# Kernel tuning notes

Hardware: AMD Instinct MI355X
Metric: run time of the kernel (lower is better)

The kernel has to match this reference:

```python
import jax, jax.numpy as jnp
import numpy as np

N_EMBED = 1024
N_HEADS = 16
HEAD_SIZE = N_EMBED // N_HEADS
B, T = 4, 2048
LN_EPS = 1e-5


def _layer_norm(x, gamma, beta):
    mu = jnp.mean(x, axis=-1, keepdims=True)
    var = jnp.var(x, axis=-1, keepdims=True)
    return (x - mu) * jax.lax.rsqrt(var + LN_EPS) * gamma + beta


def setup_inputs() -> dict:
    key = jax.random.key(0)
    ks = jax.random.split(key, 12)
    s = 1.0 / np.sqrt(N_EMBED)
    sh = 1.0 / np.sqrt(4 * N_EMBED)
    return {
        "x": jax.random.normal(ks[0], (B, T, N_EMBED), jnp.float32),
        "Wk": jax.random.uniform(ks[1], (N_EMBED, N_EMBED), jnp.float32, -s, s),
        "Wq": jax.random.uniform(ks[2], (N_EMBED, N_EMBED), jnp.float32, -s, s),
        "Wv": jax.random.uniform(ks[3], (N_EMBED, N_EMBED), jnp.float32, -s, s),
        "Wproj": jax.random.uniform(ks[4], (N_EMBED, N_EMBED), jnp.float32, -s, s),
        "bproj": jax.random.uniform(ks[5], (N_EMBED,), jnp.float32, -s, s),
        "W1": jax.random.uniform(ks[6], (N_EMBED, 4 * N_EMBED), jnp.float32, -s, s),
        "b1": jax.random.uniform(ks[7], (4 * N_EMBED,), jnp.float32, -s, s),
        "W2": jax.random.uniform(ks[8], (4 * N_EMBED, N_EMBED), jnp.float32, -sh, sh),
        "b2": jax.random.uniform(ks[9], (N_EMBED,), jnp.float32, -sh, sh),
        "g1": jnp.ones((N_EMBED,), jnp.float32),
        "beta1": jnp.zeros((N_EMBED,), jnp.float32),
        "g2": jnp.ones((N_EMBED,), jnp.float32),
        "beta2": jnp.zeros((N_EMBED,), jnp.float32),
    }


def reference(x, Wk, Wq, Wv, Wproj, bproj, W1, b1, W2, b2, g1, beta1, g2, beta2):
    Bt, Tt, C = x.shape
    h = _layer_norm(x, g1, beta1)
    # project and split heads: (B, H, T, D)
    def heads(W):
        return (h @ W).reshape(Bt, Tt, N_HEADS, HEAD_SIZE).transpose(0, 2, 1, 3)
    q, k, v = heads(Wq), heads(Wk), heads(Wv)
    wei = jnp.einsum("bhtd,bhsd->bhts", q, k) / np.sqrt(HEAD_SIZE)
    causal = jnp.tril(jnp.ones((Tt, Tt), bool))
    wei = jnp.where(causal, wei, -jnp.inf)
    wei = jax.nn.softmax(wei, axis=-1)
    out = jnp.einsum("bhts,bhsd->bhtd", wei, v)
    out = out.transpose(0, 2, 1, 3).reshape(Bt, Tt, C)
    x = x + out @ Wproj + bproj
    h2 = _layer_norm(x, g2, beta2)
    ff = jax.nn.relu(h2 @ W1 + b1) @ W2 + b2
    return x + ff
```

## Files before the change

### kernel.cpp

```cpp
#include <hip/hip_runtime.h>
#include <stdint.h>

typedef __bf16 bf16x8 __attribute__((ext_vector_type(8)));
typedef float f32x4 __attribute__((ext_vector_type(4)));
typedef unsigned short u16x8 __attribute__((ext_vector_type(8)));
typedef unsigned short u16x4 __attribute__((ext_vector_type(4)));
typedef unsigned int u32x2 __attribute__((ext_vector_type(2)));
typedef float fvec4 __attribute__((ext_vector_type(4)));

__device__ __forceinline__ unsigned short f2b(float f) {
  unsigned u = __builtin_bit_cast(unsigned, f);
  return (unsigned short)((u + 0x7fffu + ((u >> 16) & 1u)) >> 16);
}

__device__ __forceinline__ bf16x8 ldfrag(const unsigned short* p) {
  return __builtin_bit_cast(bf16x8, *(const u16x8*)p);
}

__device__ __forceinline__ float fexp2(float x) {
  float r;
  asm("v_exp_f32 %0, %1" : "=v"(r) : "v"(x));
  return r;
}

__device__ __forceinline__ unsigned cvtpk(float a, float b) {
  unsigned r;
  asm("v_cvt_pk_bf16_f32 %0, %1, %2" : "=v"(r) : "v"(a), "v"(b));
  return r;
}

__device__ __forceinline__ void gload_lds16(const void* g, void* l) {
  auto gp = reinterpret_cast<const __attribute__((address_space(1))) void*>(
      reinterpret_cast<uintptr_t>(g));
  auto lp = reinterpret_cast<__attribute__((address_space(3))) void*>(
      reinterpret_cast<uintptr_t>(l));
  __builtin_amdgcn_global_load_lds(gp, lp, 16, 0, 0);
}

__global__ void transpose_cast(const float* __restrict__ W, unsigned short* __restrict__ Wt,
                               int K, int N) {
  __shared__ float tile[32][33];
  const int n0 = blockIdx.x * 32, k0 = blockIdx.y * 32;
  const int tx = threadIdx.x, ty = threadIdx.y;
#pragma unroll
  for (int j = 0; j < 4; ++j)
    tile[ty + j * 8][tx] = W[(size_t)(k0 + ty + j * 8) * N + n0 + tx];
  __syncthreads();
#pragma unroll
  for (int j = 0; j < 4; ++j)
    Wt[(size_t)(n0 + ty + j * 8) * K + k0 + tx] = f2b(tile[tx][ty + j * 8]);
}

__global__ void ln_kernel(const float* __restrict__ X, const float* __restrict__ g,
                          const float* __restrict__ be, unsigned short* __restrict__ H) {
  const int row = (blockIdx.x * blockDim.x + threadIdx.x) >> 6;
  const int l = threadIdx.x & 63;
  const float* xr = X + (size_t)row * 1024;
  fvec4 v[4];
  float s = 0.f, sq = 0.f;
#pragma unroll
  for (int i = 0; i < 4; ++i) {
    v[i] = *(const fvec4*)(xr + i * 256 + l * 4);
#pragma unroll
    for (int j = 0; j < 4; ++j) { s += v[i][j]; sq += v[i][j] * v[i][j]; }
  }
#pragma unroll
  for (int off = 32; off >= 1; off >>= 1) {
    s += __shfl_xor(s, off);
    sq += __shfl_xor(sq, off);
  }
  const float mean = s * (1.f / 1024.f);
  const float var = sq * (1.f / 1024.f) - mean * mean;
  const float rstd = rsqrtf(var + 1e-5f);
#pragma unroll
  for (int i = 0; i < 4; ++i) {
    const int col = i * 256 + l * 4;
    fvec4 gg = *(const fvec4*)(g + col);
    fvec4 bb = *(const fvec4*)(be + col);
    u16x4 o;
#pragma unroll
    for (int j = 0; j < 4; ++j) o[j] = f2b((v[i][j] - mean) * rstd * gg[j] + bb[j]);
    *(u16x4*)(H + (size_t)row * 1024 + col) = o;
  }
}

template <int BM, int BN, int WM, int WN, int NBUF, int NTH, int EPI>
__global__ __launch_bounds__(NTH, 2) void gemm8p(
    const unsigned short* __restrict__ A, const unsigned short* __restrict__ Bt,
    const float* __restrict__ bias, const float* __restrict__ resid,
    float* __restrict__ Cf, unsigned short* __restrict__ Cb,
    unsigned short* __restrict__ pK, unsigned short* __restrict__ pVT,
    int M, int N, int K, int ntiles) {
  constexpr int BK = 32;
  constexpr int ASZ = BM * BK * 2;
  constexpr int BSZ = BN * BK * 2;
  constexpr int BUFSZ = ASZ + BSZ;
  constexpr int NW = NTH / 64;
  static_assert(WM * WN == NW, "wave grid");
  constexpr int MF = BM / (WM * 16);
  constexpr int NF = BN / (WN * 16);
  constexpr int UA = ASZ / (NTH * 16);
  constexpr int UB = BSZ / (NTH * 16);
  constexpr int UNITS = UA + UB;
  constexpr int VMSTEADY = (NBUF - 2) * UNITS;
  static_assert(UA * NTH * 16 == ASZ && UB * NTH * 16 == BSZ, "unit split");
  __shared__ __align__(16) char lds[NBUF * BUFSZ];

  const int tid = threadIdx.x;
  const int w = tid >> 6, l = tid & 63;
  const int wr = w / WN, wc = w % WN;
  const int kg = l >> 4, fr = l & 15;
  const int xtiles = N / BN;
  const int nblk = (int)gridDim.x;

  int Aoff[MF], Boff[NF];
#pragma unroll
  for (int m = 0; m < MF; ++m) {
    const int r = wr * (MF * 16) + m * 16 + fr;
    Aoff[m] = r * 64 + ((kg * 16) ^ (((r >> 1) & 3) << 4));
  }
#pragma unroll
  for (int n = 0; n < NF; ++n) {
    const int r = wc * (NF * 16) + n * 16 + fr;
    Boff[n] = ASZ + r * 64 + ((kg * 16) ^ (((r >> 1) & 3) << 4));
  }

  for (int tl = (int)blockIdx.x; tl < ntiles; tl += nblk) {
    if (tl != (int)blockIdx.x) __builtin_amdgcn_s_barrier();
    const int q8 = ntiles >> 3;
    const int swz = (tl & 7) * q8 + (tl >> 3);
    const size_t am0 = (size_t)(swz / xtiles) * BM;
    const size_t bn0 = (size_t)(swz % xtiles) * BN;

    const char* src[UNITS];
#pragma unroll
    for (int u = 0; u < UA; ++u) {
      const int flatq = u * NTH + tid;
      const int row = flatq >> 2;
      const int scb = ((flatq & 3) << 4) ^ (((row >> 1) & 3) << 4);
      src[u] = (const char*)(A + (am0 + row) * K) + scb;
    }
#pragma unroll
    for (int u = 0; u < UB; ++u) {
      const int flatq = u * NTH + tid;
      const int row = flatq >> 2;
      const int scb = ((flatq & 3) << 4) ^ (((row >> 1) & 3) << 4);
      src[UA + u] = (const char*)(Bt + (bn0 + row) * K) + scb;
    }

    f32x4 acc[MF][NF];
#pragma unroll
    for (int m = 0; m < MF; ++m)
#pragma unroll
      for (int n = 0; n < NF; ++n) acc[m][n] = (f32x4){0.f, 0.f, 0.f, 0.f};

    auto stage = [&](int sb) {
#pragma unroll
      for (int u = 0; u < UNITS; ++u) {
        gload_lds16(src[u], lds + sb * BUFSZ + u * (NTH * 16) + tid * 16);
        src[u] += 64;
      }
    };

    const int NT = K / BK;
#pragma unroll
    for (int p = 0; p < NBUF - 1; ++p) stage(p);
    asm volatile("s_waitcnt vmcnt(%0)" ::"i"(VMSTEADY) : "memory");
    __builtin_amdgcn_s_barrier();

    int cb0 = 0, sb = NBUF - 1;
    for (int kt = 0; kt < NT; ++kt) {
      if (kt + NBUF - 1 < NT) stage(sb);
      bf16x8 af[MF], bf[NF];
#pragma unroll
      for (int m = 0; m < MF; ++m)
        af[m] = ldfrag((const unsigned short*)(lds + cb0 + Aoff[m]));
#pragma unroll
      for (int n = 0; n < NF; ++n)
        bf[n] = ldfrag((const unsigned short*)(lds + cb0 + Boff[n]));
      __builtin_amdgcn_s_setprio(1);
#pragma unroll
      for (int m = 0; m < MF; ++m)
#pragma unroll
        for (int n = 0; n < NF; ++n)
          acc[m][n] = __builtin_amdgcn_mfma_f32_16x16x32_bf16(af[m], bf[n], acc[m][n], 0, 0, 0);
      __builtin_amdgcn_s_setprio(0);
      if (kt + NBUF - 1 < NT) {
        asm volatile("s_waitcnt vmcnt(%0)" ::"i"(VMSTEADY) : "memory");
        __builtin_amdgcn_s_barrier();
      } else if (kt + 2 < NT) {
        asm volatile("s_waitcnt vmcnt(%0)" ::"i"(UNITS) : "memory");
        __builtin_amdgcn_s_barrier();
      } else if (kt + 1 < NT) {
        asm volatile("s_waitcnt vmcnt(0)" ::: "memory");
        __builtin_amdgcn_s_barrier();
      }
      cb0 += BUFSZ;
      if (cb0 == NBUF * BUFSZ) cb0 = 0;
      sb += 1;
      if (sb == NBUF) sb = 0;
    }

#pragma unroll
    for (int m = 0; m < MF; ++m) {
      const size_t row0 = am0 + wr * (MF * 16) + m * 16 + kg * 4;
#pragma unroll
      for (int n = 0; n < NF; ++n) {
        const size_t col = bn0 + wc * (NF * 16) + n * 16 + fr;
        if (EPI == 3) {
          if (bn0 < 1024) {
#pragma unroll
            for (int r = 0; r < 4; ++r) Cb[(row0 + r) * 1024 + col] = f2b(acc[m][n][r]);
          } else if (bn0 < 2048) {
#pragma unroll
            for (int r = 0; r < 4; ++r) pK[(row0 + r) * 1024 + col - 1024] = f2b(acc[m][n][r]);
          } else {
            const int c2 = (int)col - 2048;
            const int hh = c2 >> 6, dd = c2 & 63;
            const int bb = (int)(row0 >> 11), tt = (int)(row0 & 2047);
            u16x4 pv;
#pragma unroll
            for (int r = 0; r < 4; ++r) pv[r] = f2b(acc[m][n][r]);
            *(u16x4*)(pVT + (((size_t)bb * 16 + hh) * 64 + dd) * 2048 + tt) = pv;
          }
        } else {
          const float bv = (EPI >= 1) ? bias[col] : 0.f;
#pragma unroll
          for (int r = 0; r < 4; ++r) {
            const size_t idx = (row0 + r) * N + col;
            float v = acc[m][n][r] + bv;
            if (EPI == 1) v = fmaxf(v, 0.f);
            if (EPI == 2) {
              Cf[idx] = v + resid[idx];
            } else {
              Cb[idx] = f2b(v);
            }
          }
        }
      }
    }
  }
}

#define PSTR 72
#define SC2 0.18033688f
__global__ __launch_bounds__(256, 2) void attn_kernel(const unsigned short* __restrict__ Qb,
                                                      const unsigned short* __restrict__ Kb,
                                                      const unsigned short* __restrict__ VT,
                                                      unsigned short* __restrict__ ATT) {
  __shared__ __align__(16) char ldsK[3 * 8192];
  __shared__ __align__(16) unsigned short Pl[4][64 * PSTR];
  const int tid = threadIdx.x;
  const int w = tid >> 6, l = tid & 63;
  const int kg = l >> 4, fr = l & 15;
  const int bh = blockIdx.x;
  const int b = bh >> 4, h = bh & 15;
  const int yy = (int)blockIdx.y;
  const int qt = (yy < 4) ? 7 - yy : yy - 4;
  const int q0 = qt * 256 + w * 64;
  const size_t rbase = (size_t)b * 2048;
  const unsigned short* vtb = VT + (size_t)bh * 64 * 2048;
  const f32x4 fz = {0.f, 0.f, 0.f, 0.f};

  const int rowoff = tid >> 3;
  const int cbsw = ((tid & 7) * 16) ^ ((rowoff & 7) << 4);
  const char* ksrc = (const char*)(Kb + rbase * 1024 + h * 64) + (size_t)rowoff * 2048 + cbsw;

  int koff[4][2];
#pragma unroll
  for (int sg = 0; sg < 4; ++sg)
#pragma unroll
    for (int c = 0; c < 2; ++c)
      koff[sg][c] = (sg * 16 + fr) * 128 + ((c * 64 + kg * 16) ^ ((fr & 7) << 4));

  bf16x8 bq[4][2];
#pragma unroll
  for (int qg = 0; qg < 4; ++qg) {
    const unsigned short* qrow = Qb + (rbase + q0 + qg * 16 + fr) * 1024 + h * 64;
#pragma unroll
    for (int c = 0; c < 2; ++c) bq[qg][c] = ldfrag(qrow + c * 32 + kg * 8);
  }

  f32x4 o[4][4];
#pragma unroll
  for (int qg = 0; qg < 4; ++qg)
#pragma unroll
    for (int nd = 0; nd < 4; ++nd) o[qg][nd] = (f32x4){0.f, 0.f, 0.f, 0.f};
  float m_run2[4] = {-1e30f, -1e30f, -1e30f, -1e30f};
  float l_run[4] = {0.f, 0.f, 0.f, 0.f};

  auto stage = [&](int t, int sbuf) {
    gload_lds16(ksrc + (size_t)(t * 64) * 2048, ldsK + sbuf * 8192 + tid * 16);
    gload_lds16(ksrc + (size_t)(t * 64 + 32) * 2048, ldsK + sbuf * 8192 + 4096 + tid * 16);
  };

  auto softmax_qg = [&](int qg, int s0, f32x4 (&stq)[4]) -> float {
    const int qa = q0 + qg * 16 + fr;
    float vals[16];
    if (s0 + 63 <= q0 + qg * 16) {
#pragma unroll
      for (int sg = 0; sg < 4; ++sg)
#pragma unroll
        for (int r = 0; r < 4; ++r) vals[sg * 4 + r] = stq[sg][r];
    } else {
#pragma unroll
      for (int sg = 0; sg < 4; ++sg)
#pragma unroll
        for (int r = 0; r < 4; ++r) {
          const int sa = s0 + sg * 16 + kg * 4 + r;
          vals[sg * 4 + r] = (sa > qa) ? -1e30f : stq[sg][r];
        }
    }
    float m5[5];
#pragma unroll
    for (int i = 0; i < 5; ++i)
      m5[i] = fmaxf(fmaxf(vals[3 * i], vals[3 * i + 1]), vals[3 * i + 2]);
    const float vmax =
        fmaxf(fmaxf(fmaxf(m5[0], m5[1]), m5[2]), fmaxf(fmaxf(m5[3], m5[4]), vals[15]));
    const float tm2 = vmax * SC2;
    if (__any(tm2 > m_run2[qg] + 8.f)) {
      float tmax2 = tm2;
      tmax2 = fmaxf(tmax2, __shfl_xor(tmax2, 16));
      tmax2 = fmaxf(tmax2, __shfl_xor(tmax2, 32));
      const float m_new2 = fmaxf(m_run2[qg], tmax2);
      const float alpha = fexp2(m_run2[qg] - m_new2);
      m_run2[qg] = m_new2;
      l_run[qg] *= alpha;
      float al[4];
#pragma unroll
      for (int r = 0; r < 4; ++r) al[r] = __shfl(alpha, kg * 4 + r);
#pragma unroll
      for (int nd = 0; nd < 4; ++nd)
#pragma unroll
        for (int r = 0; r < 4; ++r) o[qg][nd][r] *= al[r];
    }
    const float nm2 = -m_run2[qg];
    float psum = 0.f;
    unsigned pk[8];
#pragma unroll
    for (int i = 0; i < 8; ++i) {
      const float p0 = fexp2(__builtin_fmaf(vals[2 * i], SC2, nm2));
      const float p1 = fexp2(__builtin_fmaf(vals[2 * i + 1], SC2, nm2));
      psum += p0 + p1;
      pk[i] = cvtpk(p0, p1);
    }
#pragma unroll
    for (int sg = 0; sg < 4; ++sg) {
      u32x2 w2 = {pk[2 * sg], pk[2 * sg + 1]};
      *(u32x2*)(&Pl[w][(qg * 16 + fr) * PSTR + sg * 16 + kg * 4]) = w2;
    }
    return psum;
  };

  auto compute = [&](int s0, int cbb) {
    if (s0 > q0 + 63) return;
    bf16x8 vb[4][2];
#pragma unroll
    for (int nd = 0; nd < 4; ++nd)
#pragma unroll
      for (int ks = 0; ks < 2; ++ks)
        vb[nd][ks] = ldfrag(vtb + (size_t)(nd * 16 + fr) * 2048 + s0 + ks * 32 + kg * 8);

    float psv[4];
#pragma unroll
    for (int qp = 0; qp < 2; ++qp) {
      f32x4 st[4][2];
#pragma unroll
      for (int sg = 0; sg < 4; ++sg) {
        const bf16x8 ka0 = ldfrag((const unsigned short*)(ldsK + cbb + koff[sg][0]));
        const bf16x8 ka1 = ldfrag((const unsigned short*)(ldsK + cbb + koff[sg][1]));
#pragma unroll
        for (int qh = 0; qh < 2; ++qh)
          st[sg][qh] = __builtin_amdgcn_mfma_f32_16x16x32_bf16(
              ka1, bq[qp * 2 + qh][1],
              __builtin_amdgcn_mfma_f32_16x16x32_bf16(ka0, bq[qp * 2 + qh][0], fz, 0, 0, 0),
              0, 0, 0);
      }
#pragma unroll
      for (int qh = 0; qh < 2; ++qh) {
        f32x4 stq[4];
#pragma unroll
        for (int sg = 0; sg < 4; ++sg) stq[sg] = st[sg][qh];
        psv[qp * 2 + qh] = softmax_qg(qp * 2 + qh, s0, stq);
      }
    }

    {
      float a[4], c[4];
#pragma unroll
      for (int qg = 0; qg < 4; ++qg) a[qg] = __shfl_xor(psv[qg], 16);
#pragma unroll
      for (int qg = 0; qg < 4; ++qg) psv[qg] += a[qg];
#pragma unroll
      for (int qg = 0; qg < 4; ++qg) c[qg] = __shfl_xor(psv[qg], 32);
#pragma unroll
      for (int qg = 0; qg < 4; ++qg) l_run[qg] += psv[qg] + c[qg];
    }

#pragma unroll
    for (int qg = 0; qg < 4; ++qg)
#pragma unroll
      for (int ks = 0; ks < 2; ++ks) {
        const bf16x8 pa = ldfrag(&Pl[w][(qg * 16 + fr) * PSTR + ks * 32 + kg * 8]);
#pragma unroll
        for (int nd = 0; nd < 4; ++nd)
          o[qg][nd] = __builtin_amdgcn_mfma_f32_16x16x32_bf16(pa, vb[nd][ks], o[qg][nd], 0, 0, 0);
      }
  };

  const int NT = 4 * qt + 4;
  stage(0, 0);
  stage(1, 1);
  asm volatile("s_waitcnt vmcnt(2)" ::: "memory");
  __builtin_amdgcn_s_barrier();
  int cb = 0, sb = 2;
  for (int t = 0; t < NT; ++t) {
    if (t + 2 < NT) stage(t + 2, sb);
    compute(t * 64, cb * 8192);
    if (t + 2 < NT) {
      asm volatile("s_waitcnt vmcnt(2)" ::: "memory");
      __builtin_amdgcn_s_barrier();
    } else if (t + 1 < NT) {
      asm volatile("s_waitcnt vmcnt(0)" ::: "memory");
      __builtin_amdgcn_s_barrier();
    }
    cb += 1; if (cb == 3) cb = 0;
    sb += 1; if (sb == 3) sb = 0;
  }

#pragma unroll
  for (int qg = 0; qg < 4; ++qg) {
    const float li = __builtin_amdgcn_rcpf(l_run[qg]);
    float linv[4];
#pragma unroll
    for (int r = 0; r < 4; ++r) linv[r] = __shfl(li, kg * 4 + r);
#pragma unroll
    for (int nd = 0; nd < 4; ++nd)
#pragma unroll
      for (int r = 0; r < 4; ++r) {
        const size_t row = rbase + q0 + qg * 16 + kg * 4 + r;
        ATT[row * 1024 + h * 64 + nd * 16 + fr] = f2b(o[qg][nd][r] * linv[r]);
      }
  }
}

extern "C" void kernel_launch(void* const* d_in, const int* in_sizes, int n_in, void* d_out,
                              int out_size, void* d_ws, size_t ws_size, hipStream_t stream) {
  const float* x = (const float*)d_in[0];
  const float* Wk = (const float*)d_in[1];
  const float* Wq = (const float*)d_in[2];
  const float* Wv = (const float*)d_in[3];
  const float* Wproj = (const float*)d_in[4];
  const float* bproj = (const float*)d_in[5];
  const float* W1 = (const float*)d_in[6];
  const float* b1 = (const float*)d_in[7];
  const float* W2 = (const float*)d_in[8];
  const float* b2 = (const float*)d_in[9];
  const float* g1 = (const float*)d_in[10];
  const float* beta1 = (const float*)d_in[11];
  const float* g2 = (const float*)d_in[12];
  const float* beta2 = (const float*)d_in[13];
  float* out = (float*)d_out;
  unsigned short* wsu = (unsigned short*)d_ws;

  const size_t o_qkvW = 0;
  const size_t o_projW = o_qkvW + 3072 * 1024;
  const size_t o_W1 = o_projW + 1024 * 1024;
  const size_t o_W2 = o_W1 + 4096 * 1024;
  const size_t o_H = o_W2 + 1024 * 4096;
  const size_t o_Q = o_H + (size_t)8192 * 1024;
  const size_t o_K = o_Q + (size_t)8192 * 1024;
  const size_t o_VT = o_K + (size_t)8192 * 1024;
  const size_t o_ATT = o_VT + (size_t)8192 * 1024;
  const size_t o_FF1 = o_Q;

  dim3 tpb(32, 8);
  transpose_cast<<<dim3(32, 32), tpb, 0, stream>>>(Wq, wsu + o_qkvW, 1024, 1024);
  transpose_cast<<<dim3(32, 32), tpb, 0, stream>>>(Wk, wsu + o_qkvW + 1024 * 1024, 1024, 1024);
  transpose_cast<<<dim3(32, 32), tpb, 0, stream>>>(Wv, wsu + o_qkvW + 2 * 1024 * 1024, 1024, 1024);
  transpose_cast<<<dim3(32, 32), tpb, 0, stream>>>(Wproj, wsu + o_projW, 1024, 1024);
  transpose_cast<<<dim3(128, 32), tpb, 0, stream>>>(W1, wsu + o_W1, 1024, 4096);
  transpose_cast<<<dim3(32, 128), tpb, 0, stream>>>(W2, wsu + o_W2, 4096, 1024);

  ln_kernel<<<2048, 256, 0, stream>>>(x, g1, beta1, wsu + o_H);

  gemm8p<256, 128, 2, 2, 3, 256, 3><<<512, 256, 0, stream>>>(
      wsu + o_H, wsu + o_qkvW, nullptr, nullptr, nullptr, wsu + o_Q, wsu + o_K, wsu + o_VT,
      8192, 3072, 1024, 768);

  attn_kernel<<<dim3(64, 8), 256, 0, stream>>>(wsu + o_Q, wsu + o_K, wsu + o_VT, wsu + o_ATT);

  gemm8p<128, 128, 2, 2, 3, 256, 2><<<512, 256, 0, stream>>>(
      wsu + o_ATT, wsu + o_projW, bproj, x, out, nullptr, nullptr, nullptr,
      8192, 1024, 1024, 512);

  ln_kernel<<<2048, 256, 0, stream>>>(out, g2, beta2, wsu + o_H);

  gemm8p<256, 128, 2, 2, 3, 256, 1><<<512, 256, 0, stream>>>(
      wsu + o_H, wsu + o_W1, b1, nullptr, nullptr, wsu + o_FF1, nullptr, nullptr,
      8192, 4096, 1024, 1024);

  gemm8p<128, 128, 2, 2, 3, 256, 2><<<512, 256, 0, stream>>>(
      wsu + o_FF1, wsu + o_W2, b2, out, out, nullptr, nullptr, nullptr,
      8192, 1024, 4096, 512);
}
```

Measured before the change: 351.5 us.

## Replace persistent GEMM with 512-thread double-buffered BK=64 split-phase pipeline

Replaces the templated persistent 256-thread GEMM with a fixed 128x256-tile, 8-wave kernel that uses two 48 KB LDS buffers and BK=64. Each K step is split into two half-phases, and the next tile's global-to-LDS loads are issued between the fragment reads and the MFMAs, so loads overlap compute. The grid becomes one block per tile instead of a persistent loop, and occupancy drops to one block per CU. Projection and FFN2 launch only 256 blocks, which may underfill the GPU and add wave-quantization losses.

```diff
diff --git a/kernel.cpp b/kernel.cpp
--- a/kernel.cpp
+++ b/kernel.cpp
@@ -84,157 +84,186 @@
   }
 }
 
-template <int BM, int BN, int WM, int WN, int NBUF, int NTH, int EPI>
-__global__ __launch_bounds__(NTH, 2) void gemm8p(
+template <int EPI>
+__global__ __launch_bounds__(512, 1) void gemm2p(
     const unsigned short* __restrict__ A, const unsigned short* __restrict__ Bt,
     const float* __restrict__ bias, const float* __restrict__ resid,
     float* __restrict__ Cf, unsigned short* __restrict__ Cb,
-    unsigned short* __restrict__ pK, unsigned short* __restrict__ pVT,
-    int M, int N, int K, int ntiles) {
-  constexpr int BK = 32;
-  constexpr int ASZ = BM * BK * 2;
-  constexpr int BSZ = BN * BK * 2;
-  constexpr int BUFSZ = ASZ + BSZ;
-  constexpr int NW = NTH / 64;
-  static_assert(WM * WN == NW, "wave grid");
-  constexpr int MF = BM / (WM * 16);
-  constexpr int NF = BN / (WN * 16);
-  constexpr int UA = ASZ / (NTH * 16);
-  constexpr int UB = BSZ / (NTH * 16);
-  constexpr int UNITS = UA + UB;
-  constexpr int VMSTEADY = (NBUF - 2) * UNITS;
-  static_assert(UA * NTH * 16 == ASZ && UB * NTH * 16 == BSZ, "unit split");
-  __shared__ __align__(16) char lds[NBUF * BUFSZ];
-
+    unsigned short* __restrict__ pK, unsigned short* __restrict__ pVT, int N, int K) {
+  __shared__ __align__(16) char lds[2 * 49152];
   const int tid = threadIdx.x;
   const int w = tid >> 6, l = tid & 63;
-  const int wr = w / WN, wc = w % WN;
+  const int wr = w >> 2, wc = w & 3;
   const int kg = l >> 4, fr = l & 15;
-  const int xtiles = N / BN;
-  const int nblk = (int)gridDim.x;
-
-  int Aoff[MF], Boff[NF];
-#pragma unroll
-  for (int m = 0; m < MF; ++m) {
-    const int r = wr * (MF * 16) + m * 16 + fr;
-    Aoff[m] = r * 64 + ((kg * 16) ^ (((r >> 1) & 3) << 4));
-  }
-#pragma unroll
-  for (int n = 0; n < NF; ++n) {
-    const int r = wc * (NF * 16) + n * 16 + fr;
-    Boff[n] = ASZ + r * 64 + ((kg * 16) ^ (((r >> 1) & 3) << 4));
-  }
-
-  for (int tl = (int)blockIdx.x; tl < ntiles; tl += nblk) {
-    if (tl != (int)blockIdx.x) __builtin_amdgcn_s_barrier();
-    const int q8 = ntiles >> 3;
-    const int swz = (tl & 7) * q8 + (tl >> 3);
-    const size_t am0 = (size_t)(swz / xtiles) * BM;
-    const size_t bn0 = (size_t)(swz % xtiles) * BN;
-
-    const char* src[UNITS];
-#pragma unroll
-    for (int u = 0; u < UA; ++u) {
-      const int flatq = u * NTH + tid;
-      const int row = flatq >> 2;
-      const int scb = ((flatq & 3) << 4) ^ (((row >> 1) & 3) << 4);
-      src[u] = (const char*)(A + (am0 + row) * K) + scb;
-    }
-#pragma unroll
-    for (int u = 0; u < UB; ++u) {
-      const int flatq = u * NTH + tid;
-      const int row = flatq >> 2;
-      const int scb = ((flatq & 3) << 4) ^ (((row >> 1) & 3) << 4);
-      src[UA + u] = (const char*)(Bt + (bn0 + row) * K) + scb;
-    }
-
-    f32x4 acc[MF][NF];
-#pragma unroll
-    for (int m = 0; m < MF; ++m)
-#pragma unroll
-      for (int n = 0; n < NF; ++n) acc[m][n] = (f32x4){0.f, 0.f, 0.f, 0.f};
-
-    auto stage = [&](int sb) {
-#pragma unroll
-      for (int u = 0; u < UNITS; ++u) {
-        gload_lds16(src[u], lds + sb * BUFSZ + u * (NTH * 16) + tid * 16);
-        src[u] += 64;
-      }
-    };
-
-    const int NT = K / BK;
-#pragma unroll
-    for (int p = 0; p < NBUF - 1; ++p) stage(p);
-    asm volatile("s_waitcnt vmcnt(%0)" ::"i"(VMSTEADY) : "memory");
+  const int ntiles = (int)gridDim.x;
+
+  const int q8 = ntiles >> 3;
+  const int bid = (int)blockIdx.x;
+  const int swz = (bid & 7) * q8 + (bid >> 3);
+  const size_t am0 = (size_t)(swz % 64) * 128;
+  const size_t bn0 = (size_t)(swz / 64) * 256;
+
+  int Aoff[2][4], Boff[2][4];
+#pragma unroll
+  for (int kk = 0; kk < 2; ++kk) {
+#pragma unroll
+    for (int mf = 0; mf < 4; ++mf) {
+      const int r = wr * 64 + mf * 16 + fr;
+      Aoff[kk][mf] = (kk ? 24576 : 0) + r * 64 + ((kg ^ ((r >> 1) & 3)) << 4);
+    }
+#pragma unroll
+    for (int nf = 0; nf < 4; ++nf) {
+      const int rn = wc * 64 + nf * 16 + fr;
+      Boff[kk][nf] = (kk ? 32768 : 8192) + rn * 64 + ((kg ^ ((rn >> 1) & 3)) << 4);
+    }
+  }
+
+  const int rA = tid >> 2, cA = tid & 3;
+  const char* sA = (const char*)(A + (am0 + rA) * K) + ((cA ^ ((rA >> 1) & 3)) << 4);
+  const int rB0 = tid >> 2;
+  const int rB1 = 128 + (tid >> 2);
+  const char* sB0 = (const char*)(Bt + (bn0 + rB0) * K) + ((cA ^ ((rB0 >> 1) & 3)) << 4);
+  const char* sB1 = (const char*)(Bt + (bn0 + rB1) * K) + ((cA ^ ((rB1 >> 1) & 3)) << 4);
+
+  f32x4 acc[4][4];
+#pragma unroll
+  for (int m = 0; m < 4; ++m)
+#pragma unroll
+    for (int n = 0; n < 4; ++n) acc[m][n] = (f32x4){0.f, 0.f, 0.f, 0.f};
+
+  const int NT = K >> 6;
+
+  auto stage_p12 = [&](int d) {
+    char* Ld = lds + d * 49152;
+    gload_lds16(sA, Ld + tid * 16);
+    gload_lds16(sB0, Ld + 8192 + tid * 16);
+    gload_lds16(sB1, Ld + 16384 + tid * 16);
+  };
+  auto stage_p34 = [&](int d) {
+    char* Ld = lds + d * 49152;
+    gload_lds16(sA + 64, Ld + 24576 + tid * 16);
+    gload_lds16(sB0 + 64, Ld + 32768 + tid * 16);
+    gload_lds16(sB1 + 64, Ld + 40960 + tid * 16);
+  };
+
+  auto do_mfma = [&](int d, int kk) {
+    const char* Ld = lds + d * 49152;
+    bf16x8 af[4], bf[4];
+#pragma unroll
+    for (int mf = 0; mf < 4; ++mf)
+      af[mf] = ldfrag((const unsigned short*)(Ld + Aoff[kk][mf]));
+#pragma unroll
+    for (int nf = 0; nf < 4; ++nf)
+      bf[nf] = ldfrag((const unsigned short*)(Ld + Boff[kk][nf]));
     __builtin_amdgcn_s_barrier();
-
-    int cb0 = 0, sb = NBUF - 1;
-    for (int kt = 0; kt < NT; ++kt) {
-      if (kt + NBUF - 1 < NT) stage(sb);
-      bf16x8 af[MF], bf[NF];
-#pragma unroll
-      for (int m = 0; m < MF; ++m)
-        af[m] = ldfrag((const unsigned short*)(lds + cb0 + Aoff[m]));
-#pragma unroll
-      for (int n = 0; n < NF; ++n)
-        bf[n] = ldfrag((const unsigned short*)(lds + cb0 + Boff[n]));
+    asm volatile("s_waitcnt lgkmcnt(0)" ::: "memory");
+    __builtin_amdgcn_sched_barrier(0);
+    __builtin_amdgcn_s_setprio(1);
+#pragma unroll
+    for (int m = 0; m < 4; ++m)
+#pragma unroll
+      for (int n = 0; n < 4; ++n)
+        acc[m][n] = __builtin_amdgcn_mfma_f32_16x16x32_bf16(af[m], bf[n], acc[m][n], 0, 0, 0);
+    __builtin_amdgcn_s_setprio(0);
+  };
+
+  stage_p12(0);
+  stage_p34(0);
+  sA += 128; sB0 += 128; sB1 += 128;
+  asm volatile("s_waitcnt vmcnt(3)" ::: "memory");
+  __builtin_amdgcn_s_barrier();
+
+  for (int t = 0; t < NT - 1; ++t) {
+    const int d = t & 1, dn = d ^ 1;
+    {
+      const char* Ld = lds + d * 49152;
+      bf16x8 af[4], bf[4];
+#pragma unroll
+      for (int mf = 0; mf < 4; ++mf)
+        af[mf] = ldfrag((const unsigned short*)(Ld + Aoff[0][mf]));
+#pragma unroll
+      for (int nf = 0; nf < 4; ++nf)
+        bf[nf] = ldfrag((const unsigned short*)(Ld + Boff[0][nf]));
+      stage_p12(dn);
+      __builtin_amdgcn_s_barrier();
+      asm volatile("s_waitcnt lgkmcnt(0)" ::: "memory");
+      __builtin_amdgcn_sched_barrier(0);
       __builtin_amdgcn_s_setprio(1);
 #pragma unroll
-      for (int m = 0; m < MF; ++m)
-#pragma unroll
-        for (int n = 0; n < NF; ++n)
+      for (int m = 0; m < 4; ++m)
+#pragma unroll
+        for (int n = 0; n < 4; ++n)
           acc[m][n] = __builtin_amdgcn_mfma_f32_16x16x32_bf16(af[m], bf[n], acc[m][n], 0, 0, 0);
       __builtin_amdgcn_s_setprio(0);
-      if (kt + NBUF - 1 < NT) {
-        asm volatile("s_waitcnt vmcnt(%0)" ::"i"(VMSTEADY) : "memory");
-        __builtin_amdgcn_s_barrier();
-      } else if (kt + 2 < NT) {
-        asm volatile("s_waitcnt vmcnt(%0)" ::"i"(UNITS) : "memory");
-        __builtin_amdgcn_s_barrier();
-      } else if (kt + 1 < NT) {
-        asm volatile("s_waitcnt vmcnt(0)" ::: "memory");
-        __builtin_amdgcn_s_barrier();
-      }
-      cb0 += BUFSZ;
-      if (cb0 == NBUF * BUFSZ) cb0 = 0;
-      sb += 1;
-      if (sb == NBUF) sb = 0;
-    }
-
-#pragma unroll
-    for (int m = 0; m < MF; ++m) {
-      const size_t row0 = am0 + wr * (MF * 16) + m * 16 + kg * 4;
-#pragma unroll
-      for (int n = 0; n < NF; ++n) {
-        const size_t col = bn0 + wc * (NF * 16) + n * 16 + fr;
-        if (EPI == 3) {
-          if (bn0 < 1024) {
-#pragma unroll
-            for (int r = 0; r < 4; ++r) Cb[(row0 + r) * 1024 + col] = f2b(acc[m][n][r]);
-          } else if (bn0 < 2048) {
-#pragma unroll
-            for (int r = 0; r < 4; ++r) pK[(row0 + r) * 1024 + col - 1024] = f2b(acc[m][n][r]);
+      asm volatile("s_waitcnt vmcnt(3)" ::: "memory");
+      __builtin_amdgcn_s_barrier();
+    }
+    {
+      const char* Ld = lds + d * 49152;
+      bf16x8 af[4], bf[4];
+#pragma unroll
+      for (int mf = 0; mf < 4; ++mf)
+        af[mf] = ldfrag((const unsigned short*)(Ld + Aoff[1][mf]));
+#pragma unroll
+      for (int nf = 0; nf < 4; ++nf)
+        bf[nf] = ldfrag((const unsigned short*)(Ld + Boff[1][nf]));
+      stage_p34(dn);
+      sA += 128; sB0 += 128; sB1 += 128;
+      __builtin_amdgcn_s_barrier();
+      asm volatile("s_waitcnt lgkmcnt(0)" ::: "memory");
+      __builtin_amdgcn_sched_barrier(0);
+      __builtin_amdgcn_s_setprio(1);
+#pragma unroll
+      for (int m = 0; m < 4; ++m)
+#pragma unroll
+        for (int n = 0; n < 4; ++n)
+          acc[m][n] = __builtin_amdgcn_mfma_f32_16x16x32_bf16(af[m], bf[n], acc[m][n], 0, 0, 0);
+      __builtin_amdgcn_s_setprio(0);
+      asm volatile("s_waitcnt vmcnt(3)" ::: "memory");
+      __builtin_amdgcn_s_barrier();
+    }
+  }
+  {
+    const int d = (NT - 1) & 1;
+    do_mfma(d, 0);
+    asm volatile("s_waitcnt vmcnt(0)" ::: "memory");
+    __builtin_amdgcn_s_barrier();
+    do_mfma(d, 1);
+  }
+
+#pragma unroll
+  for (int m = 0; m < 4; ++m) {
+    const size_t row0 = am0 + wr * 64 + m * 16 + kg * 4;
+#pragma unroll
+    for (int n = 0; n < 4; ++n) {
+      const size_t col = bn0 + wc * 64 + n * 16 + fr;
+      if (EPI == 3) {
+        if (bn0 < 1024) {
+#pragma unroll
+          for (int r = 0; r < 4; ++r) Cb[(row0 + r) * 1024 + col] = f2b(acc[m][n][r]);
+        } else if (bn0 < 2048) {
+#pragma unroll
+          for (int r = 0; r < 4; ++r) pK[(row0 + r) * 1024 + col - 1024] = f2b(acc[m][n][r]);
+        } else {
+          const int c2 = (int)col - 2048;
+          const int hh = c2 >> 6, dd = c2 & 63;
+          const int bb = (int)(row0 >> 11), tt = (int)(row0 & 2047);
+          u16x4 pv;
+#pragma unroll
+          for (int r = 0; r < 4; ++r) pv[r] = f2b(acc[m][n][r]);
+          *(u16x4*)(pVT + (((size_t)bb * 16 + hh) * 64 + dd) * 2048 + tt) = pv;
+        }
+      } else {
+        const float bv = (EPI >= 1) ? bias[col] : 0.f;
+#pragma unroll
+        for (int r = 0; r < 4; ++r) {
+          const size_t idx = (row0 + r) * N + col;
+          float v = acc[m][n][r] + bv;
+          if (EPI == 1) v = fmaxf(v, 0.f);
+          if (EPI == 2) {
+            Cf[idx] = v + resid[idx];
           } else {
-            const int c2 = (int)col - 2048;
-            const int hh = c2 >> 6, dd = c2 & 63;
-            const int bb = (int)(row0 >> 11), tt = (int)(row0 & 2047);
-            u16x4 pv;
-#pragma unroll
-            for (int r = 0; r < 4; ++r) pv[r] = f2b(acc[m][n][r]);
-            *(u16x4*)(pVT + (((size_t)bb * 16 + hh) * 64 + dd) * 2048 + tt) = pv;
-          }
-        } else {
-          const float bv = (EPI >= 1) ? bias[col] : 0.f;
-#pragma unroll
-          for (int r = 0; r < 4; ++r) {
-            const size_t idx = (row0 + r) * N + col;
-            float v = acc[m][n][r] + bv;
-            if (EPI == 1) v = fmaxf(v, 0.f);
-            if (EPI == 2) {
-              Cf[idx] = v + resid[idx];
-            } else {
-              Cb[idx] = f2b(v);
-            }
+            Cb[idx] = f2b(v);
           }
         }
       }
@@ -484,23 +513,19 @@
 
   ln_kernel<<<2048, 256, 0, stream>>>(x, g1, beta1, wsu + o_H);
 
-  gemm8p<256, 128, 2, 2, 3, 256, 3><<<512, 256, 0, stream>>>(
-      wsu + o_H, wsu + o_qkvW, nullptr, nullptr, nullptr, wsu + o_Q, wsu + o_K, wsu + o_VT,
-      8192, 3072, 1024, 768);
+  gemm2p<3><<<768, 512, 0, stream>>>(wsu + o_H, wsu + o_qkvW, nullptr, nullptr, nullptr,
+                                     wsu + o_Q, wsu + o_K, wsu + o_VT, 3072, 1024);
 
   attn_kernel<<<dim3(64, 8), 256, 0, stream>>>(wsu + o_Q, wsu + o_K, wsu + o_VT, wsu + o_ATT);
 
-  gemm8p<128, 128, 2, 2, 3, 256, 2><<<512, 256, 0, stream>>>(
-      wsu + o_ATT, wsu + o_projW, bproj, x, out, nullptr, nullptr, nullptr,
-      8192, 1024, 1024, 512);
+  gemm2p<2><<<256, 512, 0, stream>>>(wsu + o_ATT, wsu + o_projW, bproj, x, out, nullptr,
+                                     nullptr, nullptr, 1024, 1024);
 
   ln_kernel<<<2048, 256, 0, stream>>>(out, g2, beta2, wsu + o_H);
 
-  gemm8p<256, 128, 2, 2, 3, 256, 1><<<512, 256, 0, stream>>>(
-      wsu + o_H, wsu + o_W1, b1, nullptr, nullptr, wsu + o_FF1, nullptr, nullptr,
-      8192, 4096, 1024, 1024);
-
-  gemm8p<128, 128, 2, 2, 3, 256, 2><<<512, 256, 0, stream>>>(
-      wsu + o_FF1, wsu + o_W2, b2, out, out, nullptr, nullptr, nullptr,
-      8192, 1024, 4096, 512);
-}
+  gemm2p<1><<<1024, 512, 0, stream>>>(wsu + o_H, wsu + o_W1, b1, nullptr, nullptr,
+                                      wsu + o_FF1, nullptr, nullptr, 4096, 1024);
+
+  gemm2p<2><<<256, 512, 0, stream>>>(wsu + o_FF1, wsu + o_W2, b2, out, out, nullptr,
+                                     nullptr, nullptr, 1024, 4096);
+}
```

After: 364.6 us. +3.7%, slower.

## Add 256x256-tile persistent GEMM with 4-stage pipeline for FFN1

Applied to the files above, without the earlier changes.

Adds a new GEMM kernel that computes 256x256 output tiles with 512 threads (8 waves as 2x4), a 4-buffer LDS ring with two stages prefetched, and a persistent grid of 256 blocks looping over 512 tiles in a swizzled order. It replaces the 256x128 gemm8p used for the first FFN matmul. The larger tile is meant to raise operand reuse per LDS load and cut global traffic, and persistence cuts launch tail effects. In exchange it uses 128KB of LDS at occupancy 1 and a heavy register load per wave.

```diff
diff --git a/kernel.cpp b/kernel.cpp
--- a/kernel.cpp
+++ b/kernel.cpp
@@ -242,6 +242,128 @@
   }
 }
 
+template <int EPI>
+__global__ __launch_bounds__(512, 1) void gemm44(
+    const unsigned short* __restrict__ A, const unsigned short* __restrict__ Bt,
+    const float* __restrict__ bias, const float* __restrict__ resid,
+    float* __restrict__ Cf, unsigned short* __restrict__ Cb, int N, int K, int ntiles) {
+  constexpr int BUFSZ = 32768;
+  __shared__ __align__(16) char lds[4 * BUFSZ];
+  const int tid = threadIdx.x;
+  const int w = tid >> 6, l = tid & 63;
+  const int wr = w >> 2, wc = w & 3;
+  const int kg = l >> 4, fr = l & 15;
+  const int xtiles = N / 256;
+  const int nblk = (int)gridDim.x;
+
+  int Aoff[8], Boff[4];
+#pragma unroll
+  for (int m = 0; m < 8; ++m) {
+    const int r = wr * 128 + m * 16 + fr;
+    Aoff[m] = r * 64 + ((kg ^ ((r >> 1) & 3)) << 4);
+  }
+#pragma unroll
+  for (int n = 0; n < 4; ++n) {
+    const int rn = wc * 64 + n * 16 + fr;
+    Boff[n] = 16384 + rn * 64 + ((kg ^ ((rn >> 1) & 3)) << 4);
+  }
+
+  for (int tl = (int)blockIdx.x; tl < ntiles; tl += nblk) {
+    if (tl != (int)blockIdx.x) __builtin_amdgcn_s_barrier();
+    const int q8 = ntiles >> 3;
+    const int swz = (tl & 7) * q8 + (tl >> 3);
+    const size_t am0 = (size_t)(swz / xtiles) * 256;
+    const size_t bn0 = (size_t)(swz % xtiles) * 256;
+
+    const char* src[4];
+#pragma unroll
+    for (int u = 0; u < 2; ++u) {
+      const int flat = u * 512 + tid;
+      const int row = flat >> 2;
+      const int scb = ((flat & 3) << 4) ^ (((row >> 1) & 3) << 4);
+      src[u] = (const char*)(A + (am0 + row) * K) + scb;
+    }
+#pragma unroll
+    for (int u = 0; u < 2; ++u) {
+      const int flat = u * 512 + tid;
+      const int row = flat >> 2;
+      const int scb = ((flat & 3) << 4) ^ (((row >> 1) & 3) << 4);
+      src[2 + u] = (const char*)(Bt + (bn0 + row) * K) + scb;
+    }
+
+    f32x4 acc[8][4];
+#pragma unroll
+    for (int m = 0; m < 8; ++m)
+#pragma unroll
+      for (int n = 0; n < 4; ++n) acc[m][n] = (f32x4){0.f, 0.f, 0.f, 0.f};
+
+    auto stage = [&](int sb) {
+#pragma unroll
+      for (int u = 0; u < 4; ++u) {
+        gload_lds16(src[u], lds + sb * BUFSZ + u * 8192 + tid * 16);
+        src[u] += 64;
+      }
+    };
+
+    const int NT = K >> 5;
+    stage(0);
+    stage(1);
+    asm volatile("s_waitcnt vmcnt(4)" ::: "memory");
+    __builtin_amdgcn_s_barrier();
+
+    int cb0 = 0, sb = 2;
+    for (int kt = 0; kt < NT; ++kt) {
+      if (kt + 2 < NT) stage(sb);
+      bf16x8 af[8], bf[4];
+#pragma unroll
+      for (int m = 0; m < 8; ++m)
+        af[m] = ldfrag((const unsigned short*)(lds + cb0 + Aoff[m]));
+#pragma unroll
+      for (int n = 0; n < 4; ++n)
+        bf[n] = ldfrag((const unsigned short*)(lds + cb0 + Boff[n]));
+      __builtin_amdgcn_s_setprio(1);
+#pragma unroll
+      for (int m = 0; m < 8; ++m)
+#pragma unroll
+        for (int n = 0; n < 4; ++n)
+          acc[m][n] = __builtin_amdgcn_mfma_f32_16x16x32_bf16(af[m], bf[n], acc[m][n], 0, 0, 0);
+      __builtin_amdgcn_s_setprio(0);
+      if (kt + 2 < NT) {
+        asm volatile("s_waitcnt vmcnt(4)" ::: "memory");
+        __builtin_amdgcn_s_barrier();
+      } else if (kt + 1 < NT) {
+        asm volatile("s_waitcnt vmcnt(0)" ::: "memory");
+        __builtin_amdgcn_s_barrier();
+      }
+      cb0 += BUFSZ;
+      if (cb0 == 4 * BUFSZ) cb0 = 0;
+      sb += 1;
+      if (sb == 4) sb = 0;
+    }
+
+#pragma unroll
+    for (int m = 0; m < 8; ++m) {
+      const size_t row0 = am0 + wr * 128 + m * 16 + kg * 4;
+#pragma unroll
+      for (int n = 0; n < 4; ++n) {
+        const size_t col = bn0 + wc * 64 + n * 16 + fr;
+        const float bv = (EPI >= 1) ? bias[col] : 0.f;
+#pragma unroll
+        for (int r = 0; r < 4; ++r) {
+          const size_t idx = (row0 + r) * N + col;
+          float v = acc[m][n][r] + bv;
+          if (EPI == 1) v = fmaxf(v, 0.f);
+          if (EPI == 2) {
+            Cf[idx] = v + resid[idx];
+          } else {
+            Cb[idx] = f2b(v);
+          }
+        }
+      }
+    }
+  }
+}
+
 #define PSTR 72
 #define SC2 0.18033688f
 __global__ __launch_bounds__(256, 2) void attn_kernel(const unsigned short* __restrict__ Qb,
@@ -496,9 +618,8 @@
 
   ln_kernel<<<2048, 256, 0, stream>>>(out, g2, beta2, wsu + o_H);
 
-  gemm8p<256, 128, 2, 2, 3, 256, 1><<<512, 256, 0, stream>>>(
-      wsu + o_H, wsu + o_W1, b1, nullptr, nullptr, wsu + o_FF1, nullptr, nullptr,
-      8192, 4096, 1024, 1024);
+  gemm44<1><<<256, 512, 0, stream>>>(wsu + o_H, wsu + o_W1, b1, nullptr, nullptr,
+                                     wsu + o_FF1, 4096, 1024, 512);
 
   gemm8p<128, 128, 2, 2, 3, 256, 2><<<512, 256, 0, stream>>>(
       wsu + o_FF1, wsu + o_W2, b2, out, out, nullptr, nullptr, nullptr,
```

After: 346.4 us. About the same (-1.5%).

## Replace GEMM with 512-thread 256-wide-N tile kernel using four LDS buffers

Applied to the files above, without the earlier changes.

Replaces the templated gemm8p with gemmS, a GEMM kernel that always uses a 256-column N tile and 8 waves arranged 2x4. It runs one 512-thread block per CU over a 256-block persistent grid. Each wave now computes a larger output sub-tile, which raises data reuse per LDS fragment load and reduces the number of tiles. The LDS ring grows to four buffers with prefetch two stages ahead, and the waitcnt/barrier logic is adjusted to match. In exchange, the kernel gives up two-blocks-per-CU occupancy, holds more accumulator registers per wave, and needs up to 128KB of LDS for the BM=256 variant.

```diff
diff --git a/kernel.cpp b/kernel.cpp
--- a/kernel.cpp
+++ b/kernel.cpp
@@ -84,45 +84,38 @@
   }
 }
 
-template <int BM, int BN, int WM, int WN, int NBUF, int NTH, int EPI>
-__global__ __launch_bounds__(NTH, 2) void gemm8p(
+template <int BM, int EPI>
+__global__ __launch_bounds__(512, 1) void gemmS(
     const unsigned short* __restrict__ A, const unsigned short* __restrict__ Bt,
     const float* __restrict__ bias, const float* __restrict__ resid,
     float* __restrict__ Cf, unsigned short* __restrict__ Cb,
     unsigned short* __restrict__ pK, unsigned short* __restrict__ pVT,
-    int M, int N, int K, int ntiles) {
-  constexpr int BK = 32;
-  constexpr int ASZ = BM * BK * 2;
-  constexpr int BSZ = BN * BK * 2;
+    int N, int K, int ntiles) {
+  constexpr int ASZ = BM * 64;
+  constexpr int BSZ = 16384;
   constexpr int BUFSZ = ASZ + BSZ;
-  constexpr int NW = NTH / 64;
-  static_assert(WM * WN == NW, "wave grid");
-  constexpr int MF = BM / (WM * 16);
-  constexpr int NF = BN / (WN * 16);
-  constexpr int UA = ASZ / (NTH * 16);
-  constexpr int UB = BSZ / (NTH * 16);
-  constexpr int UNITS = UA + UB;
-  constexpr int VMSTEADY = (NBUF - 2) * UNITS;
-  static_assert(UA * NTH * 16 == ASZ && UB * NTH * 16 == BSZ, "unit split");
-  __shared__ __align__(16) char lds[NBUF * BUFSZ];
+  constexpr int UA = ASZ / 8192;
+  constexpr int UNITS = UA + 2;
+  constexpr int MF = BM / 32;
+  __shared__ __align__(16) char lds[4 * BUFSZ];
 
   const int tid = threadIdx.x;
   const int w = tid >> 6, l = tid & 63;
-  const int wr = w / WN, wc = w % WN;
+  const int wr = w >> 2, wc = w & 3;
   const int kg = l >> 4, fr = l & 15;
-  const int xtiles = N / BN;
+  const int xtiles = N / 256;
   const int nblk = (int)gridDim.x;
 
-  int Aoff[MF], Boff[NF];
+  int Aoff[MF], Boff[4];
 #pragma unroll
   for (int m = 0; m < MF; ++m) {
-    const int r = wr * (MF * 16) + m * 16 + fr;
-    Aoff[m] = r * 64 + ((kg * 16) ^ (((r >> 1) & 3) << 4));
-  }
-#pragma unroll
-  for (int n = 0; n < NF; ++n) {
-    const int r = wc * (NF * 16) + n * 16 + fr;
-    Boff[n] = ASZ + r * 64 + ((kg * 16) ^ (((r >> 1) & 3) << 4));
+    const int r = wr * (BM / 2) + m * 16 + fr;
+    Aoff[m] = r * 64 + ((kg ^ ((r >> 1) & 3)) << 4);
+  }
+#pragma unroll
+  for (int n = 0; n < 4; ++n) {
+    const int rn = wc * 64 + n * 16 + fr;
+    Boff[n] = ASZ + rn * 64 + ((kg ^ ((rn >> 1) & 3)) << 4);
   }
 
   for (int tl = (int)blockIdx.x; tl < ntiles; tl += nblk) {
@@ -130,65 +123,62 @@
     const int q8 = ntiles >> 3;
     const int swz = (tl & 7) * q8 + (tl >> 3);
     const size_t am0 = (size_t)(swz / xtiles) * BM;
-    const size_t bn0 = (size_t)(swz % xtiles) * BN;
+    const size_t bn0 = (size_t)(swz % xtiles) * 256;
 
     const char* src[UNITS];
 #pragma unroll
     for (int u = 0; u < UA; ++u) {
-      const int flatq = u * NTH + tid;
-      const int row = flatq >> 2;
-      const int scb = ((flatq & 3) << 4) ^ (((row >> 1) & 3) << 4);
+      const int flat = u * 512 + tid;
+      const int row = flat >> 2;
+      const int scb = ((flat & 3) << 4) ^ (((row >> 1) & 3) << 4);
       src[u] = (const char*)(A + (am0 + row) * K) + scb;
     }
 #pragma unroll
-    for (int u = 0; u < UB; ++u) {
-      const int flatq = u * NTH + tid;
-      const int row = flatq >> 2;
-      const int scb = ((flatq & 3) << 4) ^ (((row >> 1) & 3) << 4);
+    for (int u = 0; u < 2; ++u) {
+      const int flat = u * 512 + tid;
+      const int row = flat >> 2;
+      const int scb = ((flat & 3) << 4) ^ (((row >> 1) & 3) << 4);
       src[UA + u] = (const char*)(Bt + (bn0 + row) * K) + scb;
     }
 
-    f32x4 acc[MF][NF];
+    f32x4 acc[MF][4];
 #pragma unroll
     for (int m = 0; m < MF; ++m)
 #pragma unroll
-      for (int n = 0; n < NF; ++n) acc[m][n] = (f32x4){0.f, 0.f, 0.f, 0.f};
+      for (int n = 0; n < 4; ++n) acc[m][n] = (f32x4){0.f, 0.f, 0.f, 0.f};
 
     auto stage = [&](int sb) {
 #pragma unroll
       for (int u = 0; u < UNITS; ++u) {
-        gload_lds16(src[u], lds + sb * BUFSZ + u * (NTH * 16) + tid * 16);
+        gload_lds16(src[u], lds + sb * BUFSZ + u * 8192 + tid * 16);
         src[u] += 64;
       }
     };
 
-    const int NT = K / BK;
-#pragma unroll
-    for (int p = 0; p < NBUF - 1; ++p) stage(p);
-    asm volatile("s_waitcnt vmcnt(%0)" ::"i"(VMSTEADY) : "memory");
+    const int NT = K >> 5;
+    stage(0);
+    stage(1);
+    asm volatile("s_waitcnt vmcnt(%0)" ::"i"(UNITS) : "memory");
     __builtin_amdgcn_s_barrier();
 
-    int cb0 = 0, sb = NBUF - 1;
+    int cb0 = 0, sb = 2;
     for (int kt = 0; kt < NT; ++kt) {
-      if (kt + NBUF - 1 < NT) stage(sb);
-      bf16x8 af[MF], bf[NF];
+      if (kt + 2 < NT) stage(sb);
+      bf16x8 af[MF], bf[4];
 #pragma unroll
       for (int m = 0; m < MF; ++m)
         af[m] = ldfrag((const unsigned short*)(lds + cb0 + Aoff[m]));
 #pragma unroll
-      for (int n = 0; n < NF; ++n)
+      for (int n = 0; n < 4; ++n)
         bf[n] = ldfrag((const unsigned short*)(lds + cb0 + Boff[n]));
       __builtin_amdgcn_s_setprio(1);
 #pragma unroll
       for (int m = 0; m < MF; ++m)
 #pragma unroll
-        for (int n = 0; n < NF; ++n)
+        for (int n = 0; n < 4; ++n)
           acc[m][n] = __builtin_amdgcn_mfma_f32_16x16x32_bf16(af[m], bf[n], acc[m][n], 0, 0, 0);
       __builtin_amdgcn_s_setprio(0);
-      if (kt + NBUF - 1 < NT) {
-        asm volatile("s_waitcnt vmcnt(%0)" ::"i"(VMSTEADY) : "memory");
-        __builtin_amdgcn_s_barrier();
-      } else if (kt + 2 < NT) {
+      if (kt + 2 < NT) {
         asm volatile("s_waitcnt vmcnt(%0)" ::"i"(UNITS) : "memory");
         __builtin_amdgcn_s_barrier();
       } else if (kt + 1 < NT) {
@@ -196,17 +186,17 @@
         __builtin_amdgcn_s_barrier();
       }
       cb0 += BUFSZ;
-      if (cb0 == NBUF * BUFSZ) cb0 = 0;
+      if (cb0 == 4 * BUFSZ) cb0 = 0;
       sb += 1;
-      if (sb == NBUF) sb = 0;
+      if (sb == 4) sb = 0;
     }
 
 #pragma unroll
     for (int m = 0; m < MF; ++m) {
-      const size_t row0 = am0 + wr * (MF * 16) + m * 16 + kg * 4;
-#pragma unroll
-      for (int n = 0; n < NF; ++n) {
-        const size_t col = bn0 + wc * (NF * 16) + n * 16 + fr;
+      const size_t row0 = am0 + wr * (BM / 2) + m * 16 + kg * 4;
+#pragma unroll
+      for (int n = 0; n < 4; ++n) {
+        const size_t col = bn0 + wc * 64 + n * 16 + fr;
         if (EPI == 3) {
           if (bn0 < 1024) {
 #pragma unroll
@@ -484,23 +474,19 @@
 
   ln_kernel<<<2048, 256, 0, stream>>>(x, g1, beta1, wsu + o_H);
 
-  gemm8p<256, 128, 2, 2, 3, 256, 3><<<512, 256, 0, stream>>>(
-      wsu + o_H, wsu + o_qkvW, nullptr, nullptr, nullptr, wsu + o_Q, wsu + o_K, wsu + o_VT,
-      8192, 3072, 1024, 768);
+  gemmS<128, 3><<<256, 512, 0, stream>>>(wsu + o_H, wsu + o_qkvW, nullptr, nullptr, nullptr,
+                                         wsu + o_Q, wsu + o_K, wsu + o_VT, 3072, 1024, 768);
 
   attn_kernel<<<dim3(64, 8), 256, 0, stream>>>(wsu + o_Q, wsu + o_K, wsu + o_VT, wsu + o_ATT);
 
-  gemm8p<128, 128, 2, 2, 3, 256, 2><<<512, 256, 0, stream>>>(
-      wsu + o_ATT, wsu + o_projW, bproj, x, out, nullptr, nullptr, nullptr,
-      8192, 1024, 1024, 512);
+  gemmS<128, 2><<<256, 512, 0, stream>>>(wsu + o_ATT, wsu + o_projW, bproj, x, out, nullptr,
+                                         nullptr, nullptr, 1024, 1024, 256);
 
   ln_kernel<<<2048, 256, 0, stream>>>(out, g2, beta2, wsu + o_H);
 
-  gemm8p<256, 128, 2, 2, 3, 256, 1><<<512, 256, 0, stream>>>(
-      wsu + o_H, wsu + o_W1, b1, nullptr, nullptr, wsu + o_FF1, nullptr, nullptr,
-      8192, 4096, 1024, 1024);
-
-  gemm8p<128, 128, 2, 2, 3, 256, 2><<<512, 256, 0, stream>>>(
-      wsu + o_FF1, wsu + o_W2, b2, out, out, nullptr, nullptr, nullptr,
-      8192, 1024, 4096, 512);
-}
+  gemmS<256, 1><<<256, 512, 0, stream>>>(wsu + o_H, wsu + o_W1, b1, nullptr, nullptr,
+                                         wsu + o_FF1, nullptr, nullptr, 4096, 1024, 512);
+
+  gemmS<128, 2><<<256, 512, 0, stream>>>(wsu + o_FF1, wsu + o_W2, b2, out, out, nullptr,
+                                         nullptr, nullptr, 1024, 4096, 256);
+}
```

After: 342.9 us. 2.5% less time.
